# Optimization experiments

Hardware: AMD Instinct MI355X
Metric: run time of the kernel (lower is better)

## Reference

```python
import jax, jax.numpy as jnp
import numpy as np

BIG_NUM = 1000000000.0

def setup_inputs() -> dict:
    key0 = jax.random.key(0)
    k1, k2, k3, k4 = jax.random.split(key0, 4)
    B, T, D = 64, 4096, 512
    query = jax.random.normal(k1, (B, D), dtype=jnp.float32)
    key = jax.random.normal(k2, (B, T, D), dtype=jnp.float32)
    value = jax.random.normal(k3, (B, T, D), dtype=jnp.float32)
    mask = jax.random.randint(k4, (B, T), 0, 2, dtype=jnp.int32)
    return {"query": query, "key": key, "value": value, "mask": mask}

def reference(query, key, value, mask):
    # query: [B, D], key/value: [B, T, D], mask: [B, T] (1 = keep, 0 = mask)
    D = query.shape[1]
    scale = D ** 0.5
    # energy[b, t] = key[b, t, :] . query[b, :]
    energy = jnp.einsum('btd,bd->bt', key, query) / scale
    energy = energy + (mask.astype(jnp.float32) - 1.0) * BIG_NUM
    attn = jax.nn.softmax(energy, axis=-1)          # [B, T]
    context = jnp.einsum('bt,btd->bd', attn, value)  # [B, D]
    return (context, attn)
```

## Files before the change

### kernel.cpp

```cpp
#include <hip/hip_runtime.h>
#include <math.h>

#define B 64
#define T 4096
#define D 512
#define NCH 32
#define CHT (T / NCH)

__device__ __forceinline__ float wave_sum64(float v) {
#pragma unroll
    for (int off = 32; off; off >>= 1)
        v += __shfl_xor(v, off, 64);
    return v;
}

__global__ __launch_bounds__(256) void energy_exp_kernel(const float* __restrict__ q,
                                                         const float* __restrict__ k,
                                                         const int* __restrict__ mask,
                                                         float* __restrict__ attn,
                                                         float* __restrict__ chunk_sums) {
    const float INV_SCALE = 0.04419417382415922f;

    int blk = blockIdx.x;
    int b = blk >> 6;
    int chunk = blk & 63;
    int wave = threadIdx.x >> 6;
    int lane = threadIdx.x & 63;

    const float* qb = q + b * D;
    float4 qa = *(const float4*)(qb + lane * 4);
    float4 qc = *(const float4*)(qb + 256 + lane * 4);

    int t0 = chunk * 64 + wave * 16;
    const float* kbase = k + ((size_t)b * T + t0) * D;

    int mv = (lane < 16) ? mask[b * T + t0 + lane] : 0;
    unsigned long long mbits = __ballot(mv != 0);

    int r = ((lane >> 5) & 1) | (((lane >> 4) & 1) << 1) | (((lane >> 3) & 1) << 2);
    float gsum = 0.f;

#pragma unroll
    for (int grp = 0; grp < 2; ++grp) {
        float d8[8];
#pragma unroll
        for (int rr = 0; rr < 8; ++rr) {
            int row = grp * 8 + rr;
            d8[rr] = 0.f;
            if ((mbits >> row) & 1ull) {
                const float* kr = kbase + (size_t)row * D;
                float4 ka = *(const float4*)(kr + lane * 4);
                float4 kc = *(const float4*)(kr + 256 + lane * 4);
                d8[rr] = ka.x * qa.x + ka.y * qa.y + ka.z * qa.z + ka.w * qa.w
                       + kc.x * qc.x + kc.y * qc.y + kc.z * qc.z + kc.w * qc.w;
            }
        }
        bool b5 = (lane & 32) != 0;
        float e[4];
#pragma unroll
        for (int i = 0; i < 4; ++i) {
            float u = b5 ? d8[2*i+1] : d8[2*i];
            float s = b5 ? d8[2*i]   : d8[2*i+1];
            e[i] = u + __shfl_xor(s, 32, 64);
        }
        bool b4 = (lane & 16) != 0;
        float f[2];
#pragma unroll
        for (int i = 0; i < 2; ++i) {
            float u = b4 ? e[2*i+1] : e[2*i];
            float s = b4 ? e[2*i]   : e[2*i+1];
            f[i] = u + __shfl_xor(s, 16, 64);
        }
        bool b3 = (lane & 8) != 0;
        float u = b3 ? f[1] : f[0];
        float s = b3 ? f[0] : f[1];
        float h = u + __shfl_xor(s, 8, 64);
        h += __shfl_xor(h, 4, 64);
        h += __shfl_xor(h, 2, 64);
        h += __shfl_xor(h, 1, 64);

        int row = grp * 8 + r;
        int t = t0 + row;
        float g = ((mbits >> row) & 1ull) ? __expf(h * INV_SCALE) : 0.0f;
        gsum += g;
        if ((lane & 7) == 0)
            attn[(size_t)b * T + t] = g;
    }

    float ws = wave_sum64(gsum) * 0.125f;
    __shared__ float sred[4];
    if (lane == 0) sred[wave] = ws;
    __syncthreads();
    if (threadIdx.x == 0)
        chunk_sums[blk] = (sred[0] + sred[1]) + (sred[2] + sred[3]);
}

__global__ __launch_bounds__(256) void context_partial_kernel(float* __restrict__ attn,
                                                              const float* __restrict__ v,
                                                              const float* __restrict__ chunk_sums,
                                                              float* __restrict__ partial) {
    __shared__ float sa[CHT];
    __shared__ int   sm_c[4][64];
    __shared__ float sm_a[4][64];

    int blk = blockIdx.x;
    int b = blk >> 5;
    int ch = blk & 31;
    int tid = threadIdx.x;
    int wave = tid >> 6;
    int lane = tid & 63;

    float cs = chunk_sums[b * 64 + lane];
    float denom = wave_sum64(cs);
    float inv = 1.0f / denom;

    if (tid < CHT) sa[tid] = attn[(size_t)b * T + ch * CHT + tid];
    __syncthreads();

    int par = wave >> 1;
    int dcol = ((wave & 1) * 64 + lane) * 4;

    int myrow = 2 * lane + par;
    float mya0 = sa[myrow];
    unsigned long long ball = __ballot(mya0 != 0.0f);
    int cnt = __popcll(ball);
    int pre = __popcll(ball & ((1ull << lane) - 1ull));
    if (mya0 != 0.0f) {
        sm_c[wave][pre] = myrow;
        sm_a[wave][pre] = mya0;
    }
    __syncthreads();

    int  crow = sm_c[wave][lane];
    float ca  = sm_a[wave][lane];

    const float* vb = v + ((size_t)b * T + ch * CHT) * D + dcol;

    float4 acc = {0.f, 0.f, 0.f, 0.f};
#pragma unroll 4
    for (int j = 0; j < cnt; ++j) {
        int row = __shfl(crow, j, 64);
        float a = __shfl(ca, j, 64);
        float4 vv = *(const float4*)(vb + (size_t)row * D);
        acc.x += a * vv.x; acc.y += a * vv.y;
        acc.z += a * vv.z; acc.w += a * vv.w;
    }
    acc.x *= inv; acc.y *= inv; acc.z *= inv; acc.w *= inv;
    *(float4*)(partial + ((size_t)(b * 64 + ch * 2 + par)) * D + dcol) = acc;

    if (tid < CHT)
        attn[(size_t)b * T + ch * CHT + tid] = sa[tid] * inv;
}

__global__ __launch_bounds__(256) void context_reduce_kernel(const float* __restrict__ partial,
                                                             float* __restrict__ ctx) {
    int b = blockIdx.x;
    int tid = threadIdx.x;
    int d0 = tid * 2;
    float2 acc = {0.f, 0.f};
#pragma unroll 8
    for (int j = 0; j < 64; ++j) {
        float2 p = *(const float2*)(partial + ((size_t)(b * 64 + j)) * D + d0);
        acc.x += p.x;
        acc.y += p.y;
    }
    *(float2*)(ctx + (size_t)b * D + d0) = acc;
}

extern "C" void kernel_launch(void* const* d_in, const int* in_sizes, int n_in,
                              void* d_out, int out_size, void* d_ws, size_t ws_size,
                              hipStream_t stream) {
    const float* q    = (const float*)d_in[0];
    const float* k    = (const float*)d_in[1];
    const float* v    = (const float*)d_in[2];
    const int*   mask = (const int*)d_in[3];

    float* ctx  = (float*)d_out;
    float* attn = (float*)d_out + B * D;

    float* chunk_sums = (float*)d_ws;
    float* partial    = (float*)d_ws + 8192;

    energy_exp_kernel<<<B * 64, 256, 0, stream>>>(q, k, mask, attn, chunk_sums);
    context_partial_kernel<<<B * NCH, 256, 0, stream>>>(attn, v, chunk_sums, partial);
    context_reduce_kernel<<<B, 256, 0, stream>>>(partial, ctx);
}
```

Before: 115.9 us.

## Compact unmasked key rows per wave and enlarge energy kernel chunks

The energy kernel now builds a per-wave list of unmasked rows in shared memory and processes them in dense groups of 8. This skips the dot-product reductions that were spent on masked rows. Each block now covers 128 rows, with 32 per wave, matching the context kernel's chunking, so the chunk_sums indexing changes accordingly. The context loop unroll is also raised. The shared list is written and read within a wave without an explicit barrier, and padding slots reload row 0 redundantly.

```diff
diff --git a/kernel.cpp b/kernel.cpp
--- a/kernel.cpp
+++ b/kernel.cpp
@@ -6,6 +6,7 @@
 #define D 512
 #define NCH 32
 #define CHT (T / NCH)
+#define WSTRIP 32
 
 __device__ __forceinline__ float wave_sum64(float v) {
 #pragma unroll
@@ -21,9 +22,12 @@
                                                          float* __restrict__ chunk_sums) {
     const float INV_SCALE = 0.04419417382415922f;
 
+    __shared__ int sm_list[4][WSTRIP];
+    __shared__ float sred[4];
+
     int blk = blockIdx.x;
-    int b = blk >> 6;
-    int chunk = blk & 63;
+    int b = blk >> 5;
+    int ch = blk & 31;
     int wave = threadIdx.x >> 6;
     int lane = threadIdx.x & 63;
 
@@ -31,29 +35,37 @@
     float4 qa = *(const float4*)(qb + lane * 4);
     float4 qc = *(const float4*)(qb + 256 + lane * 4);
 
-    int t0 = chunk * 64 + wave * 16;
+    int t0 = ch * CHT + wave * WSTRIP;
     const float* kbase = k + ((size_t)b * T + t0) * D;
 
-    int mv = (lane < 16) ? mask[b * T + t0 + lane] : 0;
-    unsigned long long mbits = __ballot(mv != 0);
-
-    int r = ((lane >> 5) & 1) | (((lane >> 4) & 1) << 1) | (((lane >> 3) & 1) << 2);
+    int mv = (lane < WSTRIP) ? mask[b * T + t0 + lane] : 0;
+    unsigned int mbits = (unsigned int)__ballot(mv != 0);
+    int cnt = __popc(mbits);
+    if (lane < WSTRIP) {
+        if (mv != 0) {
+            int pre = __popc(mbits & ((1u << lane) - 1u));
+            sm_list[wave][pre] = lane;
+        } else {
+            attn[(size_t)b * T + t0 + lane] = 0.0f;
+        }
+    }
+
+    int r3 = ((lane >> 5) & 1) | (((lane >> 4) & 1) << 1) | (((lane >> 3) & 1) << 2);
     float gsum = 0.f;
-
-#pragma unroll
-    for (int grp = 0; grp < 2; ++grp) {
+    int ngrp = (cnt + 7) >> 3;
+
+#pragma unroll 1
+    for (int g = 0; g < ngrp; ++g) {
         float d8[8];
 #pragma unroll
         for (int rr = 0; rr < 8; ++rr) {
-            int row = grp * 8 + rr;
-            d8[rr] = 0.f;
-            if ((mbits >> row) & 1ull) {
-                const float* kr = kbase + (size_t)row * D;
-                float4 ka = *(const float4*)(kr + lane * 4);
-                float4 kc = *(const float4*)(kr + 256 + lane * 4);
-                d8[rr] = ka.x * qa.x + ka.y * qa.y + ka.z * qa.z + ka.w * qa.w
-                       + kc.x * qc.x + kc.y * qc.y + kc.z * qc.z + kc.w * qc.w;
-            }
+            int slot = g * 8 + rr;
+            int row = sm_list[wave][slot < cnt ? slot : 0];
+            const float* kr = kbase + (size_t)row * D;
+            float4 ka = *(const float4*)(kr + lane * 4);
+            float4 kc = *(const float4*)(kr + 256 + lane * 4);
+            d8[rr] = ka.x * qa.x + ka.y * qa.y + ka.z * qa.z + ka.w * qa.w
+                   + kc.x * qc.x + kc.y * qc.y + kc.z * qc.z + kc.w * qc.w;
         }
         bool b5 = (lane & 32) != 0;
         float e[4];
@@ -79,16 +91,19 @@
         h += __shfl_xor(h, 2, 64);
         h += __shfl_xor(h, 1, 64);
 
-        int row = grp * 8 + r;
-        int t = t0 + row;
-        float g = ((mbits >> row) & 1ull) ? __expf(h * INV_SCALE) : 0.0f;
-        gsum += g;
-        if ((lane & 7) == 0)
-            attn[(size_t)b * T + t] = g;
+        int slot = g * 8 + r3;
+        float gval = 0.f;
+        if (slot < cnt) {
+            gval = __expf(h * INV_SCALE);
+            if ((lane & 7) == 0) {
+                int row = sm_list[wave][slot];
+                attn[(size_t)b * T + t0 + row] = gval;
+            }
+        }
+        gsum += gval;
     }
 
     float ws = wave_sum64(gsum) * 0.125f;
-    __shared__ float sred[4];
     if (lane == 0) sred[wave] = ws;
     __syncthreads();
     if (threadIdx.x == 0)
@@ -110,7 +125,7 @@
     int wave = tid >> 6;
     int lane = tid & 63;
 
-    float cs = chunk_sums[b * 64 + lane];
+    float cs = (lane < NCH) ? chunk_sums[b * NCH + lane] : 0.f;
     float denom = wave_sum64(cs);
     float inv = 1.0f / denom;
 
@@ -137,7 +152,7 @@
     const float* vb = v + ((size_t)b * T + ch * CHT) * D + dcol;
 
     float4 acc = {0.f, 0.f, 0.f, 0.f};
-#pragma unroll 4
+#pragma unroll 8
     for (int j = 0; j < cnt; ++j) {
         int row = __shfl(crow, j, 64);
         float a = __shfl(ca, j, 64);
@@ -181,7 +196,7 @@
     float* chunk_sums = (float*)d_ws;
     float* partial    = (float*)d_ws + 8192;
 
-    energy_exp_kernel<<<B * 64, 256, 0, stream>>>(q, k, mask, attn, chunk_sums);
+    energy_exp_kernel<<<B * NCH, 256, 0, stream>>>(q, k, mask, attn, chunk_sums);
     context_partial_kernel<<<B * NCH, 256, 0, stream>>>(attn, v, chunk_sums, partial);
     context_reduce_kernel<<<B, 256, 0, stream>>>(partial, ctx);
 }
```

New measurement: 117.5 us. No clear change (+1.3%).
